# Kernel optimization log

Measured on AMD Instinct MI355X. Metric: run time of the kernel, lower is better.

Reference implementation:

```python
import jax, jax.numpy as jnp
import numpy as np

B, N, E, D = 8, 10000, 160000, 256
H = D // 2
SLOPE = 0.2  # LeakyReLU negative slope


def setup_inputs() -> dict:
    key = jax.random.key(0)
    ks = jax.random.split(key, 8)
    node_feats = jax.random.normal(ks[0], (B, N, D), dtype=jnp.float32)
    edge_attr = jax.random.uniform(ks[1], (E, 1), dtype=jnp.float32)
    W1 = jax.random.normal(ks[2], (2 * D, H), dtype=jnp.float32) * 0.05
    b1 = jnp.zeros((H,), dtype=jnp.float32)
    W2 = jax.random.normal(ks[3], (H, 1), dtype=jnp.float32) * 0.05
    b2 = jnp.zeros((1,), dtype=jnp.float32)
    edge_index = jax.random.randint(ks[4], (2, E), 0, N, dtype=jnp.int64)
    valid_masks = jax.random.randint(ks[5], (B, N), 0, 2).astype(bool)
    return {"node_feats": node_feats, "edge_attr": edge_attr, "W1": W1, "b1": b1,
            "W2": W2, "b2": b2, "edge_index": edge_index, "valid_masks": valid_masks}


def reference(node_feats, edge_attr, W1, b1, W2, b2, edge_index, valid_masks):
    # node_feats: [B,N,D]; edge_index: [2,E] shared across batch
    d = node_feats.shape[-1]
    src, dst = edge_index[0], edge_index[1]
    # cat([src_feats, dst_feats]) @ W1 == src @ W1[:d] + dst @ W1[d:]
    # Project per-node first, then gather per-edge: avoids the [B,E,2D] concat.
    ps = jnp.einsum('bnd,dh->bnh', node_feats, W1[:d])   # [B,N,H]
    pd = jnp.einsum('bnd,dh->bnh', node_feats, W1[d:])   # [B,N,H]
    h = ps[:, src] + pd[:, dst] + b1                      # [B,E,H]
    h = jnp.where(h >= 0, h, SLOPE * h)                   # LeakyReLU(0.2)
    scores = jnp.einsum('beh,h->be', h, W2[:, 0]) + b2[0]  # [B,E]
    scores = scores * edge_attr[:, 0]                     # edge_attr multiplies pre-softmax
    w = jax.nn.softmax(scores, axis=1)                    # global softmax over all edges
    # sparse_coo(edge_index, w) @ node_feats: out[src[e]] += w[e] * feats[dst[e]]
    msg = w[..., None] * node_feats[:, dst]               # [B,E,D]
    n = node_feats.shape[1]
    agg = jax.vmap(lambda m: jax.ops.segment_sum(m, src, num_segments=n))(msg)  # [B,N,D]
    mask = valid_masks.astype(node_feats.dtype)           # [B,N]
    cnt = mask.sum(axis=1)                                # [B]
    masked_mean = (agg * mask[..., None]).sum(axis=1) / jnp.maximum(cnt, 1.0)[:, None]
    full_mean = agg.mean(axis=1)
    graph_feats = jnp.where((cnt > 0)[:, None], masked_mean, full_mean)  # [B,D]
    return graph_feats, w
```

## Files before the change

kernel.cpp:

```cpp
#include <hip/hip_runtime.h>
#include <hip/hip_bf16.h>
#include <hip/hip_fp16.h>

#define B_ 8
#define N_ 10000
#define E_ 160000
#define D_ 256
#define H_ 128
#define SLOPE 0.2f
#define NCHUNK 100

#define NB_ 64
#define EPB_ (E_ / NB_)
#define BINS_ 256
#define NPB_ (N_ / 16)
#define SUBS_ 8

#define SB_ 256
#define SEB_ (E_ / SB_)

typedef __attribute__((ext_vector_type(8))) _Float16 v8h;
typedef __attribute__((ext_vector_type(4))) _Float16 v4h;
typedef __attribute__((ext_vector_type(2))) _Float16 v2h;
typedef __attribute__((ext_vector_type(4))) float f32x4;

static __device__ __forceinline__ float dot2f(v2h a, v2h b, float c) {
#if __has_builtin(__builtin_amdgcn_fdot2)
    return __builtin_amdgcn_fdot2(a, b, c, false);
#else
    return fmaf((float)a.y, (float)b.y, fmaf((float)a.x, (float)b.x, c));
#endif
}

static __device__ __forceinline__ void block_flags(const int* __restrict__ eidx_raw,
                                                   const unsigned int* __restrict__ mask32,
                                                   int tid, int* sfl) {
    if (tid < 64) {
        unsigned long long oddnz = __ballot(eidx_raw[2 * tid + 1] != 0);
        unsigned long long mgt1  = __ballot(mask32[tid] > 1u);
        if (tid == 0) {
            sfl[0] = (oddnz == 0ull) ? 1 : 0;
            sfl[1] = (mgt1 != 0ull) ? 1 : 0;
        }
    }
    __syncthreads();
}

__global__ __launch_bounds__(256) void kprep(const int* __restrict__ eidx_raw,
                                             const unsigned char* __restrict__ mask8,
                                             const unsigned int* __restrict__ mask32,
                                             const float* __restrict__ W1,
                                             const float* __restrict__ b1,
                                             const float* __restrict__ W2,
                                             int* __restrict__ ce,
                                             unsigned char* __restrict__ cmT,
                                             __half* __restrict__ Wt,
                                             __half* __restrict__ b1h,
                                             __half* __restrict__ w2h,
                                             int* __restrict__ cnti,
                                             int* __restrict__ hpart,
                                             int* __restrict__ flagp) {
    const int tid = threadIdx.x;
    __shared__ int sfl[2];
    __shared__ int scnt[8];

    if (blockIdx.x < 1250) {
        if (tid < 8) scnt[tid] = 0;
        block_flags(eidx_raw, mask32, tid, sfl);
        const int f_e = sfl[0], f_m = sfl[1];
        const int i = blockIdx.x * 256 + tid;
        if (i < 2 * E_) ce[i] = f_e ? eidx_raw[2 * i] : eidx_raw[i];
        if (i < B_ * N_) {
            unsigned char v = f_m ? (unsigned char)(mask8[i] != 0)
                                  : (unsigned char)(mask32[i] != 0u);
            const int b = i / N_;
            const int n = i - b * N_;
            cmT[n * 8 + b] = v;
            if (v) atomicAdd(&scnt[b], 1);
        }
        if (i < 2 * 256 * 128) {
            const int f = i & 127;
            const int row = i >> 7;
            const int c = row >> 8, k = row & 255;
            Wt[((c * 128 + f) * 256) + k] = __float2half(W1[row * 128 + f]);
        }
        if (i < 128) {
            b1h[i] = __float2half(b1[i]);
            w2h[i] = __float2half(W2[i]);
        }
        __syncthreads();
        if (tid < 8 && scnt[tid]) atomicAdd(&cnti[tid], scnt[tid]);
    } else {
        block_flags(eidx_raw, mask32, tid, sfl);
        const int f_e = sfl[0];
        __shared__ int h[BINS_];
        h[tid] = 0;
        __syncthreads();
        const int hb = blockIdx.x - 1250;
        if (hb == 0 && tid == 0) flagp[0] = 0;
        const int base = hb * EPB_;
        for (int i = tid; i < EPB_; i += 256) {
            const int e = base + i;
            const int s = f_e ? eidx_raw[2 * e] : eidx_raw[e];
            const int d = f_e ? eidx_raw[2 * (E_ + e)] : eidx_raw[E_ + e];
            const int bin = (d / NPB_) * 16 + s / NPB_;
            atomicAdd(&h[bin], 1);
        }
        __syncthreads();
        hpart[hb * BINS_ + tid] = h[tid];
    }
}

__global__ __launch_bounds__(256) void k1_mfma(const float* __restrict__ X,
                                               const __half* __restrict__ Wt,
                                               __half* __restrict__ ps,
                                               __half* __restrict__ pd,
                                               const int* __restrict__ ce,
                                               const int* __restrict__ hpart,
                                               int* __restrict__ offsetG,
                                               int* __restrict__ bstart,
                                               int* __restrict__ flagp,
                                               int4* __restrict__ esort,
                                               int* __restrict__ rank) {
    const int tid = threadIdx.x;
    __shared__ __align__(16) char smem[64 * 136 * 2];

    if (blockIdx.x == 0) {
        int* cnt  = (int*)smem;
        int* excl = (int*)smem + BINS_;
        const int bin = tid;
        int c = 0;
        for (int b = 0; b < NB_; b++) c += hpart[b * BINS_ + bin];
        cnt[bin] = c;
        __syncthreads();
        if (bin == 0) {
            int r = 0;
            for (int i = 0; i < BINS_; i++) { excl[i] = r; r += cnt[i]; }
        }
        __syncthreads();
        if ((bin & 15) == 0) bstart[bin >> 4] = excl[bin];
        if (bin == 0) bstart[16] = E_;
        int run = excl[bin];
        for (int b = 0; b < NB_; b++) {
            offsetG[b * BINS_ + bin] = run;
            run += hpart[b * BINS_ + bin];
        }
        __threadfence();
        __syncthreads();
        if (tid == 0)
            __hip_atomic_store(flagp, 1, __ATOMIC_RELEASE, __HIP_MEMORY_SCOPE_AGENT);
        return;
    }

    if (blockIdx.x <= NB_) {
        if (tid == 0) {
            while (__hip_atomic_load(flagp, __ATOMIC_ACQUIRE, __HIP_MEMORY_SCOPE_AGENT) == 0)
                __builtin_amdgcn_s_sleep(2);
        }
        __syncthreads();
        int* loc = (int*)smem;
        const int sb = blockIdx.x - 1;
        loc[tid] = offsetG[sb * BINS_ + tid];
        __syncthreads();
        const int base = sb * EPB_;
        for (int i = tid; i < EPB_; i += 256) {
            const int e = base + i;
            const int s = ce[e], d = ce[E_ + e];
            const int bin = (d / NPB_) * 16 + s / NPB_;
            const int pos = atomicAdd(&loc[bin], 1);
            esort[pos] = make_int4(s, d, e, 0);
            rank[e] = pos;
        }
        return;
    }

    const int rb = blockIdx.x - (NB_ + 1);
    const int wave = tid >> 6, lane = tid & 63;
    const int quad = lane >> 4, l16 = lane & 15;
    _Float16* Xs = (_Float16*)smem;
    _Float16* T  = (_Float16*)smem;

    f32x4 acc[2][2][4];
#pragma unroll
    for (int c = 0; c < 2; c++)
#pragma unroll
        for (int i = 0; i < 2; i++)
#pragma unroll
            for (int j = 0; j < 4; j++) acc[c][i][j] = (f32x4){0.f, 0.f, 0.f, 0.f};

    const int row_base = rb * 64;
    const int sr = tid >> 3;
    const int sc = (tid & 7) * 4;

    const float* xsrc  = &X[(size_t)(row_base + sr) * 256 + sc];
    const float* xsrc2 = xsrc + 32 * 256;
    const __half* wbase = &Wt[((size_t)(wave * 32 + l16)) * 256 + quad * 8];

    float4 xa, xb;
    v8h wcur[2][2], wnxt[2][2];

    xa = *(const float4*)(xsrc);
    xb = *(const float4*)(xsrc2);
#pragma unroll
    for (int cb = 0; cb < 2; cb++)
#pragma unroll
        for (int ft = 0; ft < 2; ft++)
            wcur[cb][ft] = *(const v8h*)(wbase + (size_t)(cb * 128 + ft * 16) * 256);
    {
        v4h pa = {(_Float16)xa.x, (_Float16)xa.y, (_Float16)xa.z, (_Float16)xa.w};
        v4h pb = {(_Float16)xb.x, (_Float16)xb.y, (_Float16)xb.z, (_Float16)xb.w};
        *(v4h*)&Xs[sr * 40 + sc] = pa;
        *(v4h*)&Xs[(sr + 32) * 40 + sc] = pb;
    }
    __syncthreads();

    for (int kc = 0; kc < 8; ++kc) {
        const int cur = kc & 1;
        if (kc < 7) {
            xa = *(const float4*)(xsrc + (kc + 1) * 32);
            xb = *(const float4*)(xsrc2 + (kc + 1) * 32);
#pragma unroll
            for (int cb = 0; cb < 2; cb++)
#pragma unroll
                for (int ft = 0; ft < 2; ft++)
                    wnxt[cb][ft] = *(const v8h*)(wbase + (size_t)(cb * 128 + ft * 16) * 256 + (kc + 1) * 32);
        }
#pragma unroll
        for (int nt = 0; nt < 4; ++nt) {
            v8h xf = *(v8h*)&Xs[cur * (64 * 40) + (nt * 16 + l16) * 40 + quad * 8];
            acc[0][0][nt] = __builtin_amdgcn_mfma_f32_16x16x32_f16(wcur[0][0], xf, acc[0][0][nt], 0, 0, 0);
            acc[0][1][nt] = __builtin_amdgcn_mfma_f32_16x16x32_f16(wcur[0][1], xf, acc[0][1][nt], 0, 0, 0);
            acc[1][0][nt] = __builtin_amdgcn_mfma_f32_16x16x32_f16(wcur[1][0], xf, acc[1][0][nt], 0, 0, 0);
            acc[1][1][nt] = __builtin_amdgcn_mfma_f32_16x16x32_f16(wcur[1][1], xf, acc[1][1][nt], 0, 0, 0);
        }
        if (kc < 7) {
            const int nb = (cur ^ 1) * (64 * 40);
            v4h pa = {(_Float16)xa.x, (_Float16)xa.y, (_Float16)xa.z, (_Float16)xa.w};
            v4h pb = {(_Float16)xb.x, (_Float16)xb.y, (_Float16)xb.z, (_Float16)xb.w};
            *(v4h*)&Xs[nb + sr * 40 + sc] = pa;
            *(v4h*)&Xs[nb + (sr + 32) * 40 + sc] = pb;
#pragma unroll
            for (int cb = 0; cb < 2; cb++)
#pragma unroll
                for (int ft = 0; ft < 2; ft++)
                    wcur[cb][ft] = wnxt[cb][ft];
        }
        __syncthreads();
    }

#pragma unroll
    for (int cb = 0; cb < 2; ++cb) {
        if (cb) __syncthreads();
#pragma unroll
        for (int nt = 0; nt < 4; ++nt)
#pragma unroll
            for (int ft = 0; ft < 2; ++ft) {
                f32x4 a = acc[cb][ft][nt];
                v4h h = {(_Float16)a.x, (_Float16)a.y, (_Float16)a.z, (_Float16)a.w};
                *(v4h*)&T[(nt * 16 + l16) * 136 + wave * 32 + ft * 16 + quad * 4] = h;
            }
        __syncthreads();
        __half* outp = cb ? pd : ps;
#pragma unroll
        for (int pass = 0; pass < 4; ++pass) {
            const int r = pass * 16 + (tid >> 4);
            const int f8 = (tid & 15) * 8;
            const int R = row_base + r;
            const int b = R / N_;
            const int n = R - b * N_;
            *(float4*)(outp + ((size_t)b * N_ + n) * 128 + f8) =
                *(const float4*)&T[r * 136 + f8];
        }
    }
}

__global__ __launch_bounds__(256) void k2_scores(const __half* __restrict__ ps,
                                                 const __half* __restrict__ pd,
                                                 const int4* __restrict__ esort,
                                                 const __half* __restrict__ b1h,
                                                 const __half* __restrict__ w2h,
                                                 const float* __restrict__ b2,
                                                 const float* __restrict__ eattr,
                                                 float* __restrict__ scS) {
    const int tid = threadIdx.x;
    const int wave = tid >> 6;
    const int lane = tid & 63;
    const int bid = blockIdx.x;
    const int batch = bid & 7;
    const int e0 = (bid >> 3) * 64;

    const int hi = (lane & 7) * 16;

    v2h b1p[8], w2p[8];
    {
        const v2h* bp = (const v2h*)(b1h + hi);
        const v2h* wp = (const v2h*)(w2h + hi);
#pragma unroll
        for (int j = 0; j < 8; j++) { b1p[j] = bp[j]; w2p[j] = wp[j]; }
    }
    const float bias2 = b2[0];
    const v2h slp = {(_Float16)SLOPE, (_Float16)SLOPE};

    const __half* psb = ps + (size_t)batch * N_ * 128;
    const __half* pdb = pd + (size_t)batch * N_ * 128;
    float* scb = scS + (size_t)batch * E_;

#pragma unroll
    for (int q = 0; q < 2; q++) {
        const int e = e0 + wave * 16 + q * 8 + (lane >> 3);
        const int4 er = esort[e];
        const int src = er.x, dst = er.y, orig = er.z;

        const float4* aps = (const float4*)&psb[(size_t)src * 128 + hi];
        const float4* apd = (const float4*)&pdb[(size_t)dst * 128 + hi];
        float4 rs[2] = {aps[0], aps[1]};
        float4 rd[2] = {apd[0], apd[1]};
        const v2h* sv = (const v2h*)rs;
        const v2h* dv = (const v2h*)rd;

        float acc = 0.f;
#pragma unroll
        for (int j = 0; j < 8; j++) {
            v2h x = sv[j] + dv[j] + b1p[j];
            v2h l = __builtin_elementwise_max(x, x * slp);
            acc = dot2f(l, w2p[j], acc);
        }
        acc += __shfl_xor(acc, 1);
        acc += __shfl_xor(acc, 2);
        acc += __shfl_xor(acc, 4);

        if ((lane & 7) == 0) {
            scb[e] = (acc + bias2) * eattr[orig];
        }
    }
}

__global__ __launch_bounds__(256) void k3s_stats(const float* __restrict__ scS,
                                                 float* __restrict__ pmax,
                                                 double* __restrict__ psum) {
    const int tid = threadIdx.x;
    const int wave = tid >> 6, lane = tid & 63;
    const int base = blockIdx.x * SEB_;

    float fm[8];
#pragma unroll
    for (int j = 0; j < 8; j++) fm[j] = -3.4e38f;
    for (int i = tid; i < SEB_; i += 256) {
        const int p = base + i;
#pragma unroll
        for (int j = 0; j < 8; j++)
            fm[j] = fmaxf(fm[j], scS[(size_t)j * E_ + p]);
    }
#pragma unroll
    for (int k = 1; k <= 32; k <<= 1)
#pragma unroll
        for (int j = 0; j < 8; j++) fm[j] = fmaxf(fm[j], __shfl_xor(fm[j], k));
    __shared__ float lmax[4][8];
    if (lane == 0)
#pragma unroll
        for (int j = 0; j < 8; j++) lmax[wave][j] = fm[j];
    __syncthreads();
    float m[8];
#pragma unroll
    for (int j = 0; j < 8; j++)
        m[j] = fmaxf(fmaxf(lmax[0][j], lmax[1][j]), fmaxf(lmax[2][j], lmax[3][j]));

    double s[8];
#pragma unroll
    for (int j = 0; j < 8; j++) s[j] = 0.0;
    for (int i = tid; i < SEB_; i += 256) {
        const int p = base + i;
#pragma unroll
        for (int j = 0; j < 8; j++)
            s[j] += (double)expf(scS[(size_t)j * E_ + p] - m[j]);
    }
#pragma unroll
    for (int k = 1; k <= 32; k <<= 1)
#pragma unroll
        for (int j = 0; j < 8; j++) s[j] += __shfl_xor(s[j], k);
    __shared__ double lsum[4][8];
    if (lane == 0)
#pragma unroll
        for (int j = 0; j < 8; j++) lsum[wave][j] = s[j];
    __syncthreads();
    if (tid < 8) {
        pmax[blockIdx.x * 8 + tid] = m[tid];
        psum[blockIdx.x * 8 + tid] = lsum[0][tid] + lsum[1][tid] + lsum[2][tid] + lsum[3][tid];
    }
}

static __device__ __forceinline__ void stats_combine(const float* __restrict__ pmax,
                                                     const double* __restrict__ psum,
                                                     int tid, float* smx, float* sinvx) {
    if (tid < 64) {
        float mc[SB_ / 64][8];
        float v[8];
#pragma unroll
        for (int j = 0; j < 8; j++) v[j] = -3.4e38f;
#pragma unroll
        for (int g = 0; g < SB_ / 64; g++) {
            const float4* p4 = (const float4*)&pmax[(g * 64 + tid) * 8];
            float4 a = p4[0], b = p4[1];
            mc[g][0] = a.x; mc[g][1] = a.y; mc[g][2] = a.z; mc[g][3] = a.w;
            mc[g][4] = b.x; mc[g][5] = b.y; mc[g][6] = b.z; mc[g][7] = b.w;
#pragma unroll
            for (int j = 0; j < 8; j++) v[j] = fmaxf(v[j], mc[g][j]);
        }
#pragma unroll
        for (int k = 1; k <= 32; k <<= 1)
#pragma unroll
            for (int j = 0; j < 8; j++) v[j] = fmaxf(v[j], __shfl_xor(v[j], k));
        double z[8];
#pragma unroll
        for (int j = 0; j < 8; j++) z[j] = 0.0;
#pragma unroll
        for (int g = 0; g < SB_ / 64; g++)
#pragma unroll
            for (int j = 0; j < 8; j++)
                z[j] += psum[(g * 64 + tid) * 8 + j] * (double)expf(mc[g][j] - v[j]);
#pragma unroll
        for (int k = 1; k <= 32; k <<= 1)
#pragma unroll
            for (int j = 0; j < 8; j++) z[j] += __shfl_xor(z[j], k);
        if (tid == 0)
#pragma unroll
            for (int j = 0; j < 8; j++) { smx[j] = v[j]; sinvx[j] = (float)(1.0 / z[j]); }
    }
}

__global__ __launch_bounds__(256) void k3ef(const int4* __restrict__ esort,
                                            const float* __restrict__ scS,
                                            const unsigned char* __restrict__ cmT,
                                            const float* __restrict__ pmax,
                                            const double* __restrict__ psum,
                                            const int* __restrict__ bstart,
                                            const int* __restrict__ rank,
                                            float* __restrict__ Wpf,
                                            float* __restrict__ Wpm,
                                            float* __restrict__ wout) {
    const int tid = threadIdx.x;
    __shared__ float smx[8], sinvx[8];
    __shared__ float lWf[NPB_ * 8];
    __shared__ float lWm[NPB_ * 8];

    stats_combine(pmax, psum, tid, smx, sinvx);

    if (blockIdx.x >= 16 * SUBS_) {
        __syncthreads();
        const int e = (blockIdx.x - 16 * SUBS_) * 256 + tid;
        const int p = rank[e];
#pragma unroll
        for (int j = 0; j < 8; j++) {
            const float v = scS[(size_t)j * E_ + p];
            wout[(size_t)j * E_ + e] = expf(v - smx[j]) * sinvx[j];
        }
        return;
    }

    const int bucket = blockIdx.x / SUBS_;
    const int sub = blockIdx.x % SUBS_;

    for (int i = tid; i < NPB_ * 8; i += 256) { lWf[i] = 0.f; lWm[i] = 0.f; }
    __syncthreads();

    float m[8], inv[8];
#pragma unroll
    for (int j = 0; j < 8; j++) { m[j] = smx[j]; inv[j] = sinvx[j]; }

    const int bs = bstart[bucket], be = bstart[bucket + 1];
    const int len = be - bs;
    const int s0 = bs + (int)((long long)len * sub / SUBS_);
    const int s1 = bs + (int)((long long)len * (sub + 1) / SUBS_);
    const int nbase = bucket * NPB_;

    for (int p = s0 + tid; p < s1; p += 256) {
        const int4 er = esort[p];
        const int src = er.x;
        const int rel = er.y - nbase;
        float wv[8];
#pragma unroll
        for (int j = 0; j < 8; j++)
            wv[j] = expf(scS[(size_t)j * E_ + p] - m[j]) * inv[j];
        const unsigned long long mm = *(const unsigned long long*)&cmT[src * 8];
        float* lf = &lWf[rel * 8];
        float* lm = &lWm[rel * 8];
#pragma unroll
        for (int j = 0; j < 8; j++) {
            atomicAdd(&lf[j], wv[j]);
            if ((mm >> (8 * j)) & 1ull) atomicAdd(&lm[j], wv[j]);
        }
    }
    __syncthreads();

    float* of = Wpf + ((size_t)bucket * SUBS_ + sub) * (NPB_ * 8);
    float* om = Wpm + ((size_t)bucket * SUBS_ + sub) * (NPB_ * 8);
    for (int i = tid; i < NPB_ * 8; i += 256) { of[i] = lWf[i]; om[i] = lWm[i]; }
}

__global__ __launch_bounds__(256) void k3g_reduce(const float* __restrict__ Wpf,
                                                  const float* __restrict__ Wpm,
                                                  float* __restrict__ WfT,
                                                  float* __restrict__ WmT) {
    const int i = blockIdx.x * 256 + threadIdx.x;
    if (i >= N_ * 8) return;
    const int n = i >> 3, b = i & 7;
    const int bucket = n / NPB_;
    const int rel = n - bucket * NPB_;
    float sf = 0.f, sm = 0.f;
#pragma unroll
    for (int sub = 0; sub < SUBS_; sub++) {
        const size_t off = ((size_t)bucket * SUBS_ + sub) * (NPB_ * 8) + rel * 8 + b;
        sf += Wpf[off];
        sm += Wpm[off];
    }
    WfT[i] = sf;
    WmT[i] = sm;
}

__global__ __launch_bounds__(256) void k4b_wsum(const float* __restrict__ X,
                                                const float* __restrict__ WmT,
                                                const float* __restrict__ WfT,
                                                float* __restrict__ gpart) {
    const int c = blockIdx.x;
    const int b = blockIdx.y;
    const int tx = threadIdx.x & 63;
    const int ty = threadIdx.x >> 6;
    const int npc = N_ / NCHUNK;
    const int n0 = c * npc;

    const float4* X4 = (const float4*)(X + (size_t)b * N_ * 256);
    float4 am = {0.f, 0.f, 0.f, 0.f};
    float4 af = {0.f, 0.f, 0.f, 0.f};

    for (int n = n0 + ty; n < n0 + npc; n += 4) {
        float wm = WmT[n * 8 + b];
        float wf = WfT[n * 8 + b];
        float4 v = X4[(size_t)n * 64 + tx];
        am.x = fmaf(wm, v.x, am.x); am.y = fmaf(wm, v.y, am.y);
        am.z = fmaf(wm, v.z, am.z); am.w = fmaf(wm, v.w, am.w);
        af.x = fmaf(wf, v.x, af.x); af.y = fmaf(wf, v.y, af.y);
        af.z = fmaf(wf, v.z, af.z); af.w = fmaf(wf, v.w, af.w);
    }

    __shared__ float4 red[256];
    red[threadIdx.x] = am;
    __syncthreads();
    if (ty == 0) {
        float4 r1 = red[tx + 64], r2 = red[tx + 128], r3 = red[tx + 192];
        am.x += r1.x + r2.x + r3.x; am.y += r1.y + r2.y + r3.y;
        am.z += r1.z + r2.z + r3.z; am.w += r1.w + r2.w + r3.w;
    }
    __syncthreads();
    red[threadIdx.x] = af;
    __syncthreads();
    if (ty == 0) {
        float4 r1 = red[tx + 64], r2 = red[tx + 128], r3 = red[tx + 192];
        af.x += r1.x + r2.x + r3.x; af.y += r1.y + r2.y + r3.y;
        af.z += r1.z + r2.z + r3.z; af.w += r1.w + r2.w + r3.w;
        float4* gp4 = (float4*)gpart;
        gp4[((c * 2 + 0) * 8 + b) * 64 + tx] = am;
        gp4[((c * 2 + 1) * 8 + b) * 64 + tx] = af;
    }
}

__global__ __launch_bounds__(256) void k5_final(const float* __restrict__ gpart,
                                                const int* __restrict__ cnti,
                                                float* __restrict__ gf) {
    const int b = blockIdx.x;
    const int d = threadIdx.x;
    float sm = 0.f, sf = 0.f;
    for (int c = 0; c < NCHUNK; c++) {
        sm += gpart[((c * 2 + 0) * 8 + b) * 256 + d];
        sf += gpart[((c * 2 + 1) * 8 + b) * 256 + d];
    }
    const float cn = (float)cnti[b];
    gf[b * 256 + d] = (cn > 0.f) ? (sm / cn) : (sf / (float)N_);
}

static inline char* align16(char* p) {
    return (char*)(((uintptr_t)p + 15) & ~(uintptr_t)15);
}

extern "C" void kernel_launch(void* const* d_in, const int* in_sizes, int n_in,
                              void* d_out, int out_size, void* d_ws, size_t ws_size,
                              hipStream_t stream) {
    const float* X     = (const float*)d_in[0];
    const float* eattr = (const float*)d_in[1];
    const float* W1    = (const float*)d_in[2];
    const float* b1    = (const float*)d_in[3];
    const float* W2    = (const float*)d_in[4];
    const float* b2    = (const float*)d_in[5];
    const int*   eidx_raw = (const int*)d_in[6];
    const unsigned char* mask8 = (const unsigned char*)d_in[7];
    const unsigned int*  mask32 = (const unsigned int*)d_in[7];

    float* out  = (float*)d_out;
    float* gf   = out;
    float* wout = out + 2048;

    char* cur = (char*)d_ws;
    __half* ps_h = (__half*)cur;             cur += (size_t)N_ * 8 * 128 * 2;
    __half* pd_h = (__half*)cur;             cur += (size_t)N_ * 8 * 128 * 2;
    __half* Wt   = (__half*)cur;             cur += 2 * 128 * 256 * 2;
    int* ce      = (int*)cur;                cur += 2 * E_ * 4;
    unsigned char* cmT = (unsigned char*)cur; cur += N_ * 8;
    cur = align16(cur);
    int* cnti    = (int*)cur;                cur += 8 * 4;
    int* flagp   = (int*)cur;                cur += 4;
    cur = align16(cur);
    float* pmax  = (float*)cur;              cur += SB_ * 8 * 4;
    cur = align16(cur);
    double* psum = (double*)cur;             cur += SB_ * 8 * 8;
    float* gpart = (float*)cur;              cur += NCHUNK * 2 * 8 * 256 * 4;
    int* hpart   = (int*)cur;                cur += NB_ * BINS_ * 4;
    int* offsetG = (int*)cur;                cur += NB_ * BINS_ * 4;
    int* bstart  = (int*)cur;                cur += 32 * 4;
    cur = align16(cur);
    int4* esort  = (int4*)cur;               cur += (size_t)E_ * 16;
    int* rankB   = (int*)cur;                cur += E_ * 4;
    __half* b1h  = (__half*)cur;             cur += 128 * 2;
    __half* w2h  = (__half*)cur;             cur += 128 * 2;
    cur = align16(cur);
    float* scS   = (float*)cur;              cur += (size_t)E_ * 8 * 4;

    char* ocur = (char*)d_ws;
    float* Wpf = (float*)ocur;               ocur += (size_t)16 * SUBS_ * NPB_ * 8 * 4;
    float* Wpm = (float*)ocur;               ocur += (size_t)16 * SUBS_ * NPB_ * 8 * 4;
    float* WfT = (float*)ocur;               ocur += N_ * 8 * 4;
    float* WmT = (float*)ocur;               ocur += N_ * 8 * 4;

    hipMemsetAsync(cnti, 0, 8 * sizeof(int), stream);
    hipLaunchKernelGGL(kprep, dim3(1250 + NB_), dim3(256), 0, stream,
                       eidx_raw, mask8, mask32, W1, b1, W2,
                       ce, cmT, Wt, b1h, w2h, cnti, hpart, flagp);
    hipLaunchKernelGGL(k1_mfma, dim3(1 + NB_ + 1250), dim3(256), 0, stream,
                       X, Wt, ps_h, pd_h, ce, hpart, offsetG, bstart, flagp, esort, rankB);
    hipLaunchKernelGGL(k2_scores, dim3(E_ / 8), dim3(256), 0, stream,
                       ps_h, pd_h, esort, b1h, w2h, b2, eattr, scS);
    hipLaunchKernelGGL(k3s_stats, dim3(SB_), dim3(256), 0, stream, scS, pmax, psum);
    hipLaunchKernelGGL(k3ef, dim3(16 * SUBS_ + E_ / 256), dim3(256), 0, stream,
                       esort, scS, cmT, pmax, psum, bstart, rankB, Wpf, Wpm, wout);
    hipLaunchKernelGGL(k3g_reduce, dim3((N_ * 8 + 255) / 256), dim3(256), 0, stream,
                       Wpf, Wpm, WfT, WmT);
    hipLaunchKernelGGL(k4b_wsum, dim3(NCHUNK, 8), dim3(256), 0, stream, X, WmT, WfT, gpart);
    hipLaunchKernelGGL(k5_final, dim3(8), dim3(256), 0, stream, gpart, cnti, gf);
}
```

Measured before the change: 276.3 us.

## Merge softmax-stats, binning, reduce and final kernels using in-kernel ticket barriers

Fuses the stats, binning/normalization, per-node reduce, and weighted-sum/final kernels into two kernels. Dependent stages inside each kernel are ordered with atomic ticket counters that blocks spin on. The goal is to cut kernel launch gaps and tail idle time between dependent stages. This relies on producer blocks being scheduled before consumers (block index order), and spinning blocks occupy compute units while they wait.

```diff
diff --git a/kernel.cpp b/kernel.cpp
--- a/kernel.cpp
+++ b/kernel.cpp
@@ -19,6 +19,11 @@
 #define SB_ 256
 #define SEB_ (E_ / SB_)
 
+#define STATB_ SB_
+#define BINB_ (16 * SUBS_)
+#define NORMB_ (E_ / 256)
+#define K3GB_ ((N_ * 8 + 255) / 256)
+
 typedef __attribute__((ext_vector_type(8))) _Float16 v8h;
 typedef __attribute__((ext_vector_type(4))) _Float16 v4h;
 typedef __attribute__((ext_vector_type(2))) _Float16 v2h;
@@ -30,6 +35,19 @@
 #else
     return fmaf((float)a.y, (float)b.y, fmaf((float)a.x, (float)b.x, c));
 #endif
+}
+
+static __device__ __forceinline__ void wait_ticket(int* t, int target, int tid) {
+    if (tid == 0) {
+        while (__hip_atomic_load(t, __ATOMIC_ACQUIRE, __HIP_MEMORY_SCOPE_AGENT) < target)
+            __builtin_amdgcn_s_sleep(8);
+    }
+    __syncthreads();
+}
+static __device__ __forceinline__ void post_ticket(int* t, int tid) {
+    __threadfence();
+    __syncthreads();
+    if (tid == 0) atomicAdd(t, 1);
 }
 
 static __device__ __forceinline__ void block_flags(const int* __restrict__ eidx_raw,
@@ -59,7 +77,7 @@
                                              __half* __restrict__ w2h,
                                              int* __restrict__ cnti,
                                              int* __restrict__ hpart,
-                                             int* __restrict__ flagp) {
+                                             int* __restrict__ ctrl) {
     const int tid = threadIdx.x;
     __shared__ int sfl[2];
     __shared__ int scnt[8];
@@ -97,7 +115,7 @@
         h[tid] = 0;
         __syncthreads();
         const int hb = blockIdx.x - 1250;
-        if (hb == 0 && tid == 0) flagp[0] = 0;
+        if (hb == 0 && tid < 4) ctrl[tid] = 0;
         const int base = hb * EPB_;
         for (int i = tid; i < EPB_; i += 256) {
             const int e = base + i;
@@ -119,7 +137,7 @@
                                                const int* __restrict__ hpart,
                                                int* __restrict__ offsetG,
                                                int* __restrict__ bstart,
-                                               int* __restrict__ flagp,
+                                               int* __restrict__ ctrl,
                                                int4* __restrict__ esort,
                                                int* __restrict__ rank) {
     const int tid = threadIdx.x;
@@ -148,16 +166,12 @@
         __threadfence();
         __syncthreads();
         if (tid == 0)
-            __hip_atomic_store(flagp, 1, __ATOMIC_RELEASE, __HIP_MEMORY_SCOPE_AGENT);
+            __hip_atomic_store(&ctrl[0], 1, __ATOMIC_RELEASE, __HIP_MEMORY_SCOPE_AGENT);
         return;
     }
 
     if (blockIdx.x <= NB_) {
-        if (tid == 0) {
-            while (__hip_atomic_load(flagp, __ATOMIC_ACQUIRE, __HIP_MEMORY_SCOPE_AGENT) == 0)
-                __builtin_amdgcn_s_sleep(2);
-        }
-        __syncthreads();
+        wait_ticket(&ctrl[0], 1, tid);
         int* loc = (int*)smem;
         const int sb = blockIdx.x - 1;
         loc[tid] = offsetG[sb * BINS_ + tid];
@@ -335,60 +349,6 @@
     }
 }
 
-__global__ __launch_bounds__(256) void k3s_stats(const float* __restrict__ scS,
-                                                 float* __restrict__ pmax,
-                                                 double* __restrict__ psum) {
-    const int tid = threadIdx.x;
-    const int wave = tid >> 6, lane = tid & 63;
-    const int base = blockIdx.x * SEB_;
-
-    float fm[8];
-#pragma unroll
-    for (int j = 0; j < 8; j++) fm[j] = -3.4e38f;
-    for (int i = tid; i < SEB_; i += 256) {
-        const int p = base + i;
-#pragma unroll
-        for (int j = 0; j < 8; j++)
-            fm[j] = fmaxf(fm[j], scS[(size_t)j * E_ + p]);
-    }
-#pragma unroll
-    for (int k = 1; k <= 32; k <<= 1)
-#pragma unroll
-        for (int j = 0; j < 8; j++) fm[j] = fmaxf(fm[j], __shfl_xor(fm[j], k));
-    __shared__ float lmax[4][8];
-    if (lane == 0)
-#pragma unroll
-        for (int j = 0; j < 8; j++) lmax[wave][j] = fm[j];
-    __syncthreads();
-    float m[8];
-#pragma unroll
-    for (int j = 0; j < 8; j++)
-        m[j] = fmaxf(fmaxf(lmax[0][j], lmax[1][j]), fmaxf(lmax[2][j], lmax[3][j]));
-
-    double s[8];
-#pragma unroll
-    for (int j = 0; j < 8; j++) s[j] = 0.0;
-    for (int i = tid; i < SEB_; i += 256) {
-        const int p = base + i;
-#pragma unroll
-        for (int j = 0; j < 8; j++)
-            s[j] += (double)expf(scS[(size_t)j * E_ + p] - m[j]);
-    }
-#pragma unroll
-    for (int k = 1; k <= 32; k <<= 1)
-#pragma unroll
-        for (int j = 0; j < 8; j++) s[j] += __shfl_xor(s[j], k);
-    __shared__ double lsum[4][8];
-    if (lane == 0)
-#pragma unroll
-        for (int j = 0; j < 8; j++) lsum[wave][j] = s[j];
-    __syncthreads();
-    if (tid < 8) {
-        pmax[blockIdx.x * 8 + tid] = m[tid];
-        psum[blockIdx.x * 8 + tid] = lsum[0][tid] + lsum[1][tid] + lsum[2][tid] + lsum[3][tid];
-    }
-}
-
 static __device__ __forceinline__ void stats_combine(const float* __restrict__ pmax,
                                                      const double* __restrict__ psum,
                                                      int tid, float* smx, float* sinvx) {
@@ -428,26 +388,131 @@
     }
 }
 
-__global__ __launch_bounds__(256) void k3ef(const int4* __restrict__ esort,
-                                            const float* __restrict__ scS,
-                                            const unsigned char* __restrict__ cmT,
-                                            const float* __restrict__ pmax,
-                                            const double* __restrict__ psum,
-                                            const int* __restrict__ bstart,
-                                            const int* __restrict__ rank,
-                                            float* __restrict__ Wpf,
-                                            float* __restrict__ Wpm,
-                                            float* __restrict__ wout) {
+__global__ __launch_bounds__(256) void k3sefg(const int4* __restrict__ esort,
+                                              const float* __restrict__ scS,
+                                              const unsigned char* __restrict__ cmT,
+                                              float* __restrict__ pmax,
+                                              double* __restrict__ psum,
+                                              const int* __restrict__ bstart,
+                                              const int* __restrict__ rank,
+                                              float* __restrict__ Wpf,
+                                              float* __restrict__ Wpm,
+                                              float* __restrict__ wout,
+                                              float* __restrict__ WfT,
+                                              float* __restrict__ WmT,
+                                              int* __restrict__ ctrl) {
     const int tid = threadIdx.x;
+    int* st_ticket  = &ctrl[1];
+    int* bin_ticket = &ctrl[2];
+
     __shared__ float smx[8], sinvx[8];
     __shared__ float lWf[NPB_ * 8];
     __shared__ float lWm[NPB_ * 8];
 
-    stats_combine(pmax, psum, tid, smx, sinvx);
-
-    if (blockIdx.x >= 16 * SUBS_) {
-        __syncthreads();
-        const int e = (blockIdx.x - 16 * SUBS_) * 256 + tid;
+    if (blockIdx.x < STATB_) {
+        const int wave = tid >> 6, lane = tid & 63;
+        const int base = blockIdx.x * SEB_;
+        float fm[8];
+#pragma unroll
+        for (int j = 0; j < 8; j++) fm[j] = -3.4e38f;
+        for (int i = tid; i < SEB_; i += 256) {
+            const int p = base + i;
+#pragma unroll
+            for (int j = 0; j < 8; j++)
+                fm[j] = fmaxf(fm[j], scS[(size_t)j * E_ + p]);
+        }
+#pragma unroll
+        for (int k = 1; k <= 32; k <<= 1)
+#pragma unroll
+            for (int j = 0; j < 8; j++) fm[j] = fmaxf(fm[j], __shfl_xor(fm[j], k));
+        __shared__ float lmax[4][8];
+        if (lane == 0)
+#pragma unroll
+            for (int j = 0; j < 8; j++) lmax[wave][j] = fm[j];
+        __syncthreads();
+        float m[8];
+#pragma unroll
+        for (int j = 0; j < 8; j++)
+            m[j] = fmaxf(fmaxf(lmax[0][j], lmax[1][j]), fmaxf(lmax[2][j], lmax[3][j]));
+
+        double s[8];
+#pragma unroll
+        for (int j = 0; j < 8; j++) s[j] = 0.0;
+        for (int i = tid; i < SEB_; i += 256) {
+            const int p = base + i;
+#pragma unroll
+            for (int j = 0; j < 8; j++)
+                s[j] += (double)expf(scS[(size_t)j * E_ + p] - m[j]);
+        }
+#pragma unroll
+        for (int k = 1; k <= 32; k <<= 1)
+#pragma unroll
+            for (int j = 0; j < 8; j++) s[j] += __shfl_xor(s[j], k);
+        __shared__ double lsum[4][8];
+        if (lane == 0)
+#pragma unroll
+            for (int j = 0; j < 8; j++) lsum[wave][j] = s[j];
+        __syncthreads();
+        if (tid < 8) {
+            pmax[blockIdx.x * 8 + tid] = m[tid];
+            psum[blockIdx.x * 8 + tid] = lsum[0][tid] + lsum[1][tid] + lsum[2][tid] + lsum[3][tid];
+        }
+        post_ticket(st_ticket, tid);
+        return;
+    }
+
+    if (blockIdx.x < STATB_ + BINB_) {
+        wait_ticket(st_ticket, STATB_, tid);
+        stats_combine(pmax, psum, tid, smx, sinvx);
+
+        const int bb = blockIdx.x - STATB_;
+        const int bucket = bb / SUBS_;
+        const int sub = bb % SUBS_;
+
+        for (int i = tid; i < NPB_ * 8; i += 256) { lWf[i] = 0.f; lWm[i] = 0.f; }
+        __syncthreads();
+
+        float m[8], inv[8];
+#pragma unroll
+        for (int j = 0; j < 8; j++) { m[j] = smx[j]; inv[j] = sinvx[j]; }
+
+        const int bs = bstart[bucket], be = bstart[bucket + 1];
+        const int len = be - bs;
+        const int s0 = bs + (int)((long long)len * sub / SUBS_);
+        const int s1 = bs + (int)((long long)len * (sub + 1) / SUBS_);
+        const int nbase = bucket * NPB_;
+
+        for (int p = s0 + tid; p < s1; p += 256) {
+            const int4 er = esort[p];
+            const int src = er.x;
+            const int rel = er.y - nbase;
+            float wv[8];
+#pragma unroll
+            for (int j = 0; j < 8; j++)
+                wv[j] = expf(scS[(size_t)j * E_ + p] - m[j]) * inv[j];
+            const unsigned long long mm = *(const unsigned long long*)&cmT[src * 8];
+            float* lf = &lWf[rel * 8];
+            float* lm = &lWm[rel * 8];
+#pragma unroll
+            for (int j = 0; j < 8; j++) {
+                atomicAdd(&lf[j], wv[j]);
+                if ((mm >> (8 * j)) & 1ull) atomicAdd(&lm[j], wv[j]);
+            }
+        }
+        __syncthreads();
+
+        float* of = Wpf + ((size_t)bucket * SUBS_ + sub) * (NPB_ * 8);
+        float* om = Wpm + ((size_t)bucket * SUBS_ + sub) * (NPB_ * 8);
+        for (int i = tid; i < NPB_ * 8; i += 256) { of[i] = lWf[i]; om[i] = lWm[i]; }
+        post_ticket(bin_ticket, tid);
+        return;
+    }
+
+    if (blockIdx.x < STATB_ + BINB_ + NORMB_) {
+        wait_ticket(st_ticket, STATB_, tid);
+        stats_combine(pmax, psum, tid, smx, sinvx);
+        __syncthreads();
+        const int e = (blockIdx.x - STATB_ - BINB_) * 256 + tid;
         const int p = rank[e];
 #pragma unroll
         for (int j = 0; j < 8; j++) {
@@ -457,51 +522,8 @@
         return;
     }
 
-    const int bucket = blockIdx.x / SUBS_;
-    const int sub = blockIdx.x % SUBS_;
-
-    for (int i = tid; i < NPB_ * 8; i += 256) { lWf[i] = 0.f; lWm[i] = 0.f; }
-    __syncthreads();
-
-    float m[8], inv[8];
-#pragma unroll
-    for (int j = 0; j < 8; j++) { m[j] = smx[j]; inv[j] = sinvx[j]; }
-
-    const int bs = bstart[bucket], be = bstart[bucket + 1];
-    const int len = be - bs;
-    const int s0 = bs + (int)((long long)len * sub / SUBS_);
-    const int s1 = bs + (int)((long long)len * (sub + 1) / SUBS_);
-    const int nbase = bucket * NPB_;
-
-    for (int p = s0 + tid; p < s1; p += 256) {
-        const int4 er = esort[p];
-        const int src = er.x;
-        const int rel = er.y - nbase;
-        float wv[8];
-#pragma unroll
-        for (int j = 0; j < 8; j++)
-            wv[j] = expf(scS[(size_t)j * E_ + p] - m[j]) * inv[j];
-        const unsigned long long mm = *(const unsigned long long*)&cmT[src * 8];
-        float* lf = &lWf[rel * 8];
-        float* lm = &lWm[rel * 8];
-#pragma unroll
-        for (int j = 0; j < 8; j++) {
-            atomicAdd(&lf[j], wv[j]);
-            if ((mm >> (8 * j)) & 1ull) atomicAdd(&lm[j], wv[j]);
-        }
-    }
-    __syncthreads();
-
-    float* of = Wpf + ((size_t)bucket * SUBS_ + sub) * (NPB_ * 8);
-    float* om = Wpm + ((size_t)bucket * SUBS_ + sub) * (NPB_ * 8);
-    for (int i = tid; i < NPB_ * 8; i += 256) { of[i] = lWf[i]; om[i] = lWm[i]; }
-}
-
-__global__ __launch_bounds__(256) void k3g_reduce(const float* __restrict__ Wpf,
-                                                  const float* __restrict__ Wpm,
-                                                  float* __restrict__ WfT,
-                                                  float* __restrict__ WmT) {
-    const int i = blockIdx.x * 256 + threadIdx.x;
+    wait_ticket(bin_ticket, BINB_, tid);
+    const int i = (blockIdx.x - STATB_ - BINB_ - NORMB_) * 256 + tid;
     if (i >= N_ * 8) return;
     const int n = i >> 3, b = i & 7;
     const int bucket = n / NPB_;
@@ -517,14 +539,34 @@
     WmT[i] = sm;
 }
 
-__global__ __launch_bounds__(256) void k4b_wsum(const float* __restrict__ X,
-                                                const float* __restrict__ WmT,
-                                                const float* __restrict__ WfT,
-                                                float* __restrict__ gpart) {
-    const int c = blockIdx.x;
-    const int b = blockIdx.y;
-    const int tx = threadIdx.x & 63;
-    const int ty = threadIdx.x >> 6;
+__global__ __launch_bounds__(256) void k4b5(const float* __restrict__ X,
+                                            const float* __restrict__ WmT,
+                                            const float* __restrict__ WfT,
+                                            const int* __restrict__ cnti,
+                                            float* __restrict__ gpart,
+                                            int* __restrict__ ctrl,
+                                            float* __restrict__ gf) {
+    const int tid = threadIdx.x;
+    int* wsum_ticket = &ctrl[3];
+
+    if (blockIdx.x >= NCHUNK * 8) {
+        wait_ticket(wsum_ticket, NCHUNK * 8, tid);
+        const int b = blockIdx.x - NCHUNK * 8;
+        const int d = tid;
+        float sm = 0.f, sf = 0.f;
+        for (int c = 0; c < NCHUNK; c++) {
+            sm += gpart[((c * 2 + 0) * 8 + b) * 256 + d];
+            sf += gpart[((c * 2 + 1) * 8 + b) * 256 + d];
+        }
+        const float cn = (float)cnti[b];
+        gf[b * 256 + d] = (cn > 0.f) ? (sm / cn) : (sf / (float)N_);
+        return;
+    }
+
+    const int c = blockIdx.x >> 3;
+    const int b = blockIdx.x & 7;
+    const int tx = tid & 63;
+    const int ty = tid >> 6;
     const int npc = N_ / NCHUNK;
     const int n0 = c * npc;
 
@@ -543,7 +585,7 @@
     }
 
     __shared__ float4 red[256];
-    red[threadIdx.x] = am;
+    red[tid] = am;
     __syncthreads();
     if (ty == 0) {
         float4 r1 = red[tx + 64], r2 = red[tx + 128], r3 = red[tx + 192];
@@ -551,7 +593,7 @@
         am.z += r1.z + r2.z + r3.z; am.w += r1.w + r2.w + r3.w;
     }
     __syncthreads();
-    red[threadIdx.x] = af;
+    red[tid] = af;
     __syncthreads();
     if (ty == 0) {
         float4 r1 = red[tx + 64], r2 = red[tx + 128], r3 = red[tx + 192];
@@ -561,20 +603,7 @@
         gp4[((c * 2 + 0) * 8 + b) * 64 + tx] = am;
         gp4[((c * 2 + 1) * 8 + b) * 64 + tx] = af;
     }
-}
-
-__global__ __launch_bounds__(256) void k5_final(const float* __restrict__ gpart,
-                                                const int* __restrict__ cnti,
-                                                float* __restrict__ gf) {
-    const int b = blockIdx.x;
-    const int d = threadIdx.x;
-    float sm = 0.f, sf = 0.f;
-    for (int c = 0; c < NCHUNK; c++) {
-        sm += gpart[((c * 2 + 0) * 8 + b) * 256 + d];
-        sf += gpart[((c * 2 + 1) * 8 + b) * 256 + d];
-    }
-    const float cn = (float)cnti[b];
-    gf[b * 256 + d] = (cn > 0.f) ? (sm / cn) : (sf / (float)N_);
+    post_ticket(wsum_ticket, tid);
 }
 
 static inline char* align16(char* p) {
@@ -606,7 +635,7 @@
     unsigned char* cmT = (unsigned char*)cur; cur += N_ * 8;
     cur = align16(cur);
     int* cnti    = (int*)cur;                cur += 8 * 4;
-    int* flagp   = (int*)cur;                cur += 4;
+    int* ctrl    = (int*)cur;                cur += 4 * 4;
     cur = align16(cur);
     float* pmax  = (float*)cur;              cur += SB_ * 8 * 4;
     cur = align16(cur);
@@ -632,16 +661,13 @@
     hipMemsetAsync(cnti, 0, 8 * sizeof(int), stream);
     hipLaunchKernelGGL(kprep, dim3(1250 + NB_), dim3(256), 0, stream,
                        eidx_raw, mask8, mask32, W1, b1, W2,
-                       ce, cmT, Wt, b1h, w2h, cnti, hpart, flagp);
+                       ce, cmT, Wt, b1h, w2h, cnti, hpart, ctrl);
     hipLaunchKernelGGL(k1_mfma, dim3(1 + NB_ + 1250), dim3(256), 0, stream,
-                       X, Wt, ps_h, pd_h, ce, hpart, offsetG, bstart, flagp, esort, rankB);
+                       X, Wt, ps_h, pd_h, ce, hpart, offsetG, bstart, ctrl, esort, rankB);
     hipLaunchKernelGGL(k2_scores, dim3(E_ / 8), dim3(256), 0, stream,
                        ps_h, pd_h, esort, b1h, w2h, b2, eattr, scS);
-    hipLaunchKernelGGL(k3s_stats, dim3(SB_), dim3(256), 0, stream, scS, pmax, psum);
-    hipLaunchKernelGGL(k3ef, dim3(16 * SUBS_ + E_ / 256), dim3(256), 0, stream,
-                       esort, scS, cmT, pmax, psum, bstart, rankB, Wpf, Wpm, wout);
-    hipLaunchKernelGGL(k3g_reduce, dim3((N_ * 8 + 255) / 256), dim3(256), 0, stream,
-                       Wpf, Wpm, WfT, WmT);
-    hipLaunchKernelGGL(k4b_wsum, dim3(NCHUNK, 8), dim3(256), 0, stream, X, WmT, WfT, gpart);
-    hipLaunchKernelGGL(k5_final, dim3(8), dim3(256), 0, stream, gpart, cnti, gf);
-}
+    hipLaunchKernelGGL(k3sefg, dim3(STATB_ + BINB_ + NORMB_ + K3GB_), dim3(256), 0, stream,
+                       esort, scS, cmT, pmax, psum, bstart, rankB, Wpf, Wpm, wout, WfT, WmT, ctrl);
+    hipLaunchKernelGGL(k4b5, dim3(NCHUNK * 8 + 8), dim3(256), 0, stream,
+                       X, WmT, WfT, cnti, gpart, ctrl, gf);
+}
```

After: 464.5 us. 1.68x slower.
